# Kernel tuning notes

Measured on AMD Instinct MI355X. Metric: run time of the kernel, lower is better.

## Reference

```python
import jax, jax.numpy as jnp
import numpy as np

B, T, D, N, L = 8, 2048, 256, 64, 4
LN_EPS = 1e-5


def setup_inputs() -> dict:
    key = jax.random.key(0)
    ks = jax.random.split(key, 8)
    def rn(k, shape, scale=1.0):
        return jax.random.normal(k, shape, dtype=jnp.float32) * scale
    A_init = jnp.log(0.5 + jnp.arange(N, dtype=jnp.float32))  # (N,)
    inp = {
        "sequences": rn(ks[0], (B, T, D)),
        # per-layer stacked params (leading dim L)
        "Wi": rn(ks[1], (L, D, D), 1.0 / np.sqrt(D)),
        "bi": jnp.zeros((L, D), jnp.float32),
        "A_log": jnp.broadcast_to(A_init, (L, D, N)) + 0.0,
        "Cm": rn(ks[2], (L, D, N), 1.0 / np.sqrt(N)),
        "Dp": jnp.ones((L, D), jnp.float32),
        "log_dt": jax.random.uniform(ks[3], (L, D), jnp.float32) * (np.log(0.1) - np.log(0.001)) + np.log(0.001),
        "Wo": rn(ks[4], (L, D, D), 1.0 / np.sqrt(D)),
        "bo": jnp.zeros((L, D), jnp.float32),
        "ln1_g": jnp.ones((L, D), jnp.float32),
        "ln1_b": jnp.zeros((L, D), jnp.float32),
        "ln2_g": jnp.ones((L, D), jnp.float32),
        "ln2_b": jnp.zeros((L, D), jnp.float32),
        "W1": rn(ks[5], (L, D, 4 * D), 1.0 / np.sqrt(D)),
        "b1": jnp.zeros((L, 4 * D), jnp.float32),
        "W2": rn(ks[6], (L, 4 * D, D), 1.0 / np.sqrt(4 * D)),
        "b2": jnp.zeros((L, D), jnp.float32),
        "lnf_g": jnp.ones((D,), jnp.float32),
        "lnf_b": jnp.zeros((D,), jnp.float32),
    }
    return inp


def _ln(x, g, b):
    m = x.mean(-1, keepdims=True)
    v = x.var(-1, keepdims=True)
    return (x - m) / jnp.sqrt(v + LN_EPS) * g + b


def _s4_kernel(A_log_l, Cm_l, log_dt_l, Tlen):
    dt = jnp.exp(log_dt_l)                       # (D,)
    A = -jnp.exp(A_log_l)                        # (D,N)
    A_bar = jnp.exp(A * dt[:, None])             # (D,N)
    B_bar = (A_bar - 1.0) / (A * np.sqrt(N))     # (D,N)
    CB = Cm_l * B_bar                            # (D,N)
    logAb = jnp.log(jnp.clip(A_bar, 1e-10))
    powers = jnp.arange(Tlen, dtype=jnp.float32)
    # (D,N,T) power tensor contracted over N -> (D,T)
    return jnp.einsum('dn,dnt->dt', CB, jnp.exp(logAb[:, :, None] * powers))


def reference(sequences, Wi, bi, A_log, Cm, Dp, log_dt, Wo, bo,
              ln1_g, ln1_b, ln2_g, ln2_b, W1, b1, W2, b2, lnf_g, lnf_b):
    x = sequences  # dropout is identity in eval mode
    Tlen = x.shape[1]
    nfft = 2 * Tlen
    for l in range(L):
        # --- S4D sub-block (pre-norm) ---
        h = _ln(x, ln1_g[l], ln1_b[l])
        u = (h @ Wi[l] + bi[l]).transpose(0, 2, 1)   # (B,D,T)
        K = _s4_kernel(A_log[l], Cm[l], log_dt[l], Tlen)  # (D,T)
        u_f = jnp.fft.rfft(u, n=nfft, axis=-1)
        K_f = jnp.fft.rfft(K, n=nfft, axis=-1)
        y = jnp.fft.irfft(u_f * K_f[None], n=nfft, axis=-1)[..., :Tlen]
        y = y + Dp[l][None, :, None] * u
        y = y.transpose(0, 2, 1) @ Wo[l] + bo[l]
        x = x + y
        # --- MLP sub-block (pre-norm) ---
        h2 = _ln(x, ln2_g[l], ln2_b[l])
        x = x + (jax.nn.gelu(h2 @ W1[l] + b1[l], approximate=False) @ W2[l] + b2[l])
    return _ln(x, lnf_g, lnf_b)
```

## Files before the change

kernel.cpp:

```cpp
#include <hip/hip_runtime.h>
#include <hip/hip_bf16.h>

#define NB 8
#define TT 2048
#define DD 256
#define NN 64
#define LL 4
#define CC 32
#define GG 64
#define BT (NB*TT)

typedef __attribute__((ext_vector_type(8))) short short8;
typedef __attribute__((ext_vector_type(4))) short short4v;
typedef __attribute__((ext_vector_type(4))) float f32x4;

__device__ __forceinline__ float bf2f(__hip_bfloat16 v){ return __bfloat162float(v); }
__device__ __forceinline__ __hip_bfloat16 f2bf(float v){ return __float2bfloat16(v); }
__device__ __forceinline__ short f2bfbits(float v){
  __hip_bfloat16 h = __float2bfloat16(v);
  return __builtin_bit_cast(short, h);
}
__device__ __forceinline__ float bfbits2f(short s){
  __hip_bfloat16 h = __builtin_bit_cast(__hip_bfloat16, s);
  return __bfloat162float(h);
}

__device__ __forceinline__ int get_bf(const void* dtp){
  unsigned u = *(const unsigned*)dtp;
  return ((u >> 16) == (u & 0xFFFFu)) ? 1 : 0;
}

__device__ __forceinline__ float ldin(const void* p, size_t i, int bf){
  return bf ? __bfloat162float(((const __hip_bfloat16*)p)[i]) : ((const float*)p)[i];
}

__device__ __forceinline__ float gelu_f(float x){
  float y = 0.79788456f * fmaf(0.044715f, x*x*x, x);
  float e = __expf(-2.0f * fabsf(y));
  float t = (1.0f - e) / (1.0f + e);
  t = (y >= 0.0f) ? t : -t;
  return 0.5f * x * (1.0f + t);
}

__device__ __forceinline__ void async16(const void* g, void* l){
  __builtin_amdgcn_global_load_lds(
      (const __attribute__((address_space(1))) void*)(unsigned long long)g,
      (__attribute__((address_space(3))) void*)(unsigned long long)l,
      16, 0, 0);
}

__global__ __launch_bounds__(256) void cast_ln_kernel(const void* __restrict__ seq,
    __hip_bfloat16* __restrict__ x, __hip_bfloat16* __restrict__ hN,
    const void* __restrict__ g, const void* __restrict__ b,
    const void* __restrict__ dtp)
{
  int bf = get_bf(dtp);
  int lane = threadIdx.x & 63, w = threadIdx.x >> 6;
  int row = blockIdx.x * 4 + w;
  int c = lane * 4;
  size_t base = (size_t)row*DD + c;
  float v0 = ldin(seq, base+0, bf), v1 = ldin(seq, base+1, bf);
  float v2 = ldin(seq, base+2, bf), v3 = ldin(seq, base+3, bf);
  short4v xk; xk.x=f2bfbits(v0); xk.y=f2bfbits(v1); xk.z=f2bfbits(v2); xk.w=f2bfbits(v3);
  *(short4v*)(x + base) = xk;
  float s = v0+v1+v2+v3;
  #pragma unroll
  for (int o = 1; o < 64; o <<= 1) s += __shfl_xor(s, o);
  float mean = s * (1.0f/DD);
  float d0=v0-mean, d1=v1-mean, d2=v2-mean, d3=v3-mean;
  float sq = d0*d0+d1*d1+d2*d2+d3*d3;
  #pragma unroll
  for (int o = 1; o < 64; o <<= 1) sq += __shfl_xor(sq, o);
  float r = rsqrtf(sq * (1.0f/DD) + 1e-5f);
  short4v hk;
  hk.x = f2bfbits(d0*r*ldin(g,c+0,bf) + ldin(b,c+0,bf));
  hk.y = f2bfbits(d1*r*ldin(g,c+1,bf) + ldin(b,c+1,bf));
  hk.z = f2bfbits(d2*r*ldin(g,c+2,bf) + ldin(b,c+2,bf));
  hk.w = f2bfbits(d3*r*ldin(g,c+3,bf) + ldin(b,c+3,bf));
  *(short4v*)(hN + base) = hk;
}

__global__ __launch_bounds__(256) void transpose_all_kernel(
    const void* __restrict__ Wi, const void* __restrict__ Wo,
    const void* __restrict__ W1, const void* __restrict__ W2,
    __hip_bfloat16* __restrict__ WiT, __hip_bfloat16* __restrict__ WoT,
    __hip_bfloat16* __restrict__ W1T, __hip_bfloat16* __restrict__ W2T,
    const void* __restrict__ dtp)
{
  int bf = get_bf(dtp);
  __shared__ float tile[32][33];
  int id = blockIdx.x;
  const void* W; __hip_bfloat16* Wt; int K, N, l, n0, k0;
  if (id < 256){
    W=Wi; Wt=WiT; K=DD; N=DD;
    int t=id;       l=t>>6; int r=t&63;  n0=(r&7)*32;  k0=(r>>3)*32;
  } else if (id < 512){
    W=Wo; Wt=WoT; K=DD; N=DD;
    int t=id-256;   l=t>>6; int r=t&63;  n0=(r&7)*32;  k0=(r>>3)*32;
  } else if (id < 1536){
    W=W1; Wt=W1T; K=DD; N=4*DD;
    int t=id-512;   l=t>>8; int r=t&255; n0=(r&31)*32; k0=(r>>5)*32;
  } else {
    W=W2; Wt=W2T; K=4*DD; N=DD;
    int t=id-1536;  l=t>>8; int r=t&255; n0=(r&7)*32;  k0=(r>>3)*32;
  }
  size_t zoff = (size_t)l * K * N;
  int tx = threadIdx.x, ty = threadIdx.y;
  #pragma unroll
  for (int i = 0; i < 4; i++)
    tile[ty + i*8][tx] = ldin(W, zoff + (size_t)(k0 + ty + i*8)*N + n0 + tx, bf);
  __syncthreads();
  #pragma unroll
  for (int i = 0; i < 4; i++)
    Wt[zoff + (size_t)(n0 + ty + i*8)*K + k0 + tx] = f2bf(tile[tx][ty + i*8]);
}

__global__ __launch_bounds__(256) void gemm_w1_kernel(
    const __hip_bfloat16* __restrict__ A, const __hip_bfloat16* __restrict__ Wt,
    const void* __restrict__ bias, size_t boff,
    __hip_bfloat16* __restrict__ C, int N, int K, const void* __restrict__ dtp)
{
  int bf = get_bf(dtp);
  __shared__ __align__(16) char smem[24576];
  short (*Als)[128][32] = (short(*)[128][32])smem;
  short (*Bls)[64][32]  = (short(*)[64][32])(smem + 16384);
  short* Cls = (short*)smem;
  int tid = threadIdx.x;
  int lane = tid & 63, w = tid >> 6;
  int quad = lane >> 4, row16 = lane & 15;
  int wm = (w >> 1) * 64, wn = (w & 1) * 32;
  int bm = blockIdx.x * 128, bn = blockIdx.y * 64;
  const short* Ag = (const short*)A + (size_t)bm * K;
  const short* Bg = (const short*)Wt + (size_t)bn * K;
  int r0 = tid >> 2, c8 = (tid & 3) * 8;
  f32x4 acc[4][2] = {};
  for (int k0 = 0; k0 < K; k0 += 64){
    #pragma unroll
    for (int kc = 0; kc < 2; kc++){
      async16(Ag + (size_t)r0*K      + k0 + kc*32 + c8, &Als[kc][r0][c8]);
      async16(Ag + (size_t)(64+r0)*K + k0 + kc*32 + c8, &Als[kc][64+r0][c8]);
      async16(Bg + (size_t)r0*K      + k0 + kc*32 + c8, &Bls[kc][r0][c8]);
    }
    __syncthreads();
    #pragma unroll
    for (int kc = 0; kc < 2; kc++){
      short8 af[4], bfr[2];
      #pragma unroll
      for (int i = 0; i < 4; i++)
        af[i] = *(const short8*)&Als[kc][wm + i*16 + row16][quad*8];
      #pragma unroll
      for (int j = 0; j < 2; j++)
        bfr[j] = *(const short8*)&Bls[kc][wn + j*16 + row16][quad*8];
      #pragma unroll
      for (int i = 0; i < 4; i++)
        #pragma unroll
        for (int j = 0; j < 2; j++)
          acc[i][j] = __builtin_amdgcn_mfma_f32_16x16x32_bf16(af[i], bfr[j], acc[i][j], 0, 0, 0);
    }
    __syncthreads();
  }
  #pragma unroll
  for (int i = 0; i < 4; i++){
    #pragma unroll
    for (int j = 0; j < 2; j++){
      int col = wn + j*16 + row16;
      float bv = ldin(bias, boff + bn + col, bf);
      #pragma unroll
      for (int r = 0; r < 4; r++){
        int row = wm + i*16 + quad*4 + r;
        Cls[row*72 + col] = f2bfbits(gelu_f(acc[i][j][r] + bv));
      }
    }
  }
  __syncthreads();
  #pragma unroll
  for (int p = 0; p < 4; p++){
    int ch = p*256 + tid;
    int row = ch >> 3, c0 = (ch & 7) * 8;
    short8 v = *(const short8*)&Cls[row*72 + c0];
    *(short8*)&C[(size_t)(bm + row)*N + bn + c0] = v;
  }
}

__global__ __launch_bounds__(256) void gemm_wi_lf_kernel(
    const __hip_bfloat16* __restrict__ A, const __hip_bfloat16* __restrict__ Wt,
    const void* __restrict__ bias, size_t boff,
    __hip_bfloat16* __restrict__ uout, __hip_bfloat16* __restrict__ LFS,
    const float* __restrict__ abT, int K, const void* __restrict__ dtp)
{
  int bf = get_bf(dtp);
  __shared__ __align__(16) char smem[73728];
  short (*Als)[2][32][32]  = (short(*)[2][32][32])smem;
  short (*Bls)[2][256][32] = (short(*)[2][256][32])(smem + 8192);
  float* Cls = (float*)smem;
  int tid = threadIdx.x, lane = tid & 63, w = tid >> 6;
  int quad = lane >> 4, row16 = lane & 15;
  int wn = w * 64;
  int bm = blockIdx.x * 32;
  const short* Ag = (const short*)A + (size_t)bm * K;
  const short* Bg = (const short*)Wt;
  int nt = K >> 6;
  {
    int ch = tid; int kc = ch>>7, r=(ch>>2)&31, c=(ch&3)*8;
    async16(Ag + (size_t)r*K + kc*32 + c, &Als[0][kc][r][c]);
    #pragma unroll
    for (int p = 0; p < 8; p++){
      int c2 = p*256 + tid; int k2 = c2>>10, r2=(c2>>2)&255, cc=(c2&3)*8;
      async16(Bg + (size_t)r2*K + k2*32 + cc, &Bls[0][k2][r2][cc]);
    }
  }
  __syncthreads();
  f32x4 acc[2][4] = {};
  for (int t = 0; t < nt; t++){
    int cur = t & 1;
    if (t + 1 < nt){
      int nb_ = cur ^ 1, k0 = (t+1) << 6;
      int ch = tid; int kc = ch>>7, r=(ch>>2)&31, c=(ch&3)*8;
      async16(Ag + (size_t)r*K + k0 + kc*32 + c, &Als[nb_][kc][r][c]);
      #pragma unroll
      for (int p = 0; p < 8; p++){
        int c2 = p*256 + tid; int k2 = c2>>10, r2=(c2>>2)&255, cc=(c2&3)*8;
        async16(Bg + (size_t)r2*K + k0 + k2*32 + cc, &Bls[nb_][k2][r2][cc]);
      }
    }
    #pragma unroll
    for (int kc = 0; kc < 2; kc++){
      short8 af[2], bfr[4];
      #pragma unroll
      for (int i = 0; i < 2; i++)
        af[i] = *(const short8*)&Als[cur][kc][i*16 + row16][quad*8];
      #pragma unroll
      for (int j = 0; j < 4; j++)
        bfr[j] = *(const short8*)&Bls[cur][kc][wn + j*16 + row16][quad*8];
      #pragma unroll
      for (int i = 0; i < 2; i++)
        #pragma unroll
        for (int j = 0; j < 4; j++)
          acc[i][j] = __builtin_amdgcn_mfma_f32_16x16x32_bf16(af[i], bfr[j], acc[i][j], 0, 0, 0);
    }
    __syncthreads();
  }
  #pragma unroll
  for (int i = 0; i < 2; i++)
    #pragma unroll
    for (int j = 0; j < 4; j++){
      int col = wn + j*16 + row16;
      #pragma unroll
      for (int r = 0; r < 4; r++){
        int row = i*16 + quad*4 + r;
        Cls[row*260 + col] = acc[i][j][r];
      }
    }
  __syncthreads();
  {
    int row = tid >> 3, l7 = tid & 7;
    size_t rbase = (size_t)(bm + row)*DD;
    #pragma unroll
    for (int q = 0; q < 8; q++){
      int c0 = l7*4 + q*32;
      float4 t = *(const float4*)&Cls[row*260 + c0];
      float v0 = t.x + ldin(bias, boff+c0+0, bf);
      float v1 = t.y + ldin(bias, boff+c0+1, bf);
      float v2 = t.z + ldin(bias, boff+c0+2, bf);
      float v3 = t.w + ldin(bias, boff+c0+3, bf);
      float4 wbk; wbk.x=v0; wbk.y=v1; wbk.z=v2; wbk.w=v3;
      *(float4*)&Cls[row*260 + c0] = wbk;
      short4v pk; pk.x=f2bfbits(v0); pk.y=f2bfbits(v1); pk.z=f2bfbits(v2); pk.w=f2bfbits(v3);
      *(short4v*)&uout[rbase + c0] = pk;
    }
  }
  __syncthreads();
  {
    int d = tid;
    int cix = bm >> 5;
    float ab[NN], accn[NN];
    #pragma unroll
    for (int n = 0; n < NN; n++){ ab[n] = abT[n*DD + d]; accn[n] = 0.0f; }
    #pragma unroll 1
    for (int s = 0; s < CC; s++){
      float uv = Cls[s*260 + d];
      #pragma unroll
      for (int n = 0; n < NN; n++) accn[n] = fmaf(ab[n], accn[n], uv);
    }
    #pragma unroll
    for (int n = 0; n < NN; n++)
      LFS[((size_t)cix*NN + n)*DD + d] = f2bf(accn[n]);
  }
}

__global__ __launch_bounds__(256) void s4_scan_kernel(__hip_bfloat16* __restrict__ LFS,
    const float* __restrict__ AbarCT)
{
  int d = threadIdx.x;
  int n = blockIdx.x & (NN-1), b = blockIdx.x >> 6;
  float a = AbarCT[n*DD + d];
  size_t base = ((size_t)(b*GG)*NN + n)*DD + d;
  const size_t gs = (size_t)NN*DD;
  float s = 0.0f;
  #pragma unroll 1
  for (int g = 0; g < GG; g += 4){
    size_t i0 = base + (size_t)(g+0)*gs;
    size_t i1 = base + (size_t)(g+1)*gs;
    size_t i2 = base + (size_t)(g+2)*gs;
    size_t i3 = base + (size_t)(g+3)*gs;
    float lf0 = bf2f(LFS[i0]);
    float lf1 = bf2f(LFS[i1]);
    float lf2 = bf2f(LFS[i2]);
    float lf3 = bf2f(LFS[i3]);
    LFS[i0] = f2bf(s); s = fmaf(a, s, lf0);
    LFS[i1] = f2bf(s); s = fmaf(a, s, lf1);
    LFS[i2] = f2bf(s); s = fmaf(a, s, lf2);
    LFS[i3] = f2bf(s); s = fmaf(a, s, lf3);
  }
}

__global__ __launch_bounds__(512, 4) void gemm_wo_recur_kernel(
    const __hip_bfloat16* __restrict__ uB, const __hip_bfloat16* __restrict__ Sin,
    const float* __restrict__ abT, const float* __restrict__ cbT,
    const void* __restrict__ Dp, size_t dpoff,
    const __hip_bfloat16* __restrict__ Wt, const void* __restrict__ bias, size_t boff,
    const __hip_bfloat16* __restrict__ resx, __hip_bfloat16* __restrict__ xout,
    const void* __restrict__ g, size_t goff, const void* __restrict__ bb, size_t bboff,
    __hip_bfloat16* __restrict__ hout)
{
  int bf = get_bf(Dp);
  __shared__ __align__(16) char smem[50176];
  short* Uls   = (short*)smem;
  short* Afull = (short*)(smem + 16384);
  short* Bext  = (short*)(smem + 32768);
  float* Cls   = (float*)(smem + 16384);
  int tid = threadIdx.x, lane = tid & 63, w = tid >> 6;
  int quad = lane >> 4, row16 = lane & 15;
  int bm = blockIdx.x * CC;
  const short* Bg = (const short*)Wt;
  {
    const short* ug = (const short*)uB + (size_t)bm * DD;
    async16(ug + tid*8,        Uls + tid*8);
    async16(ug + 4096 + tid*8, Uls + 4096 + tid*8);
    #pragma unroll
    for (int p = 0; p < 2; p++){
      int ch = p*512 + tid; int r = ch >> 2, c = (ch & 3) * 8;
      async16(Bg + (size_t)r*DD + c, Bext + ch*8);
    }
  }
  int d = tid >> 1, ng = tid & 1, nb = ng * 32;
  float st[32], ab[32], cb[32];
  {
    const __hip_bfloat16* sbase = Sin + ((size_t)(bm >> 5) * NN + nb)*DD + d;
    const float* abase = abT + (size_t)nb*DD + d;
    const float* cbase = cbT + (size_t)nb*DD + d;
    #pragma unroll
    for (int i = 0; i < 32; i++){
      st[i] = bf2f(sbase[(size_t)i*DD]);
      ab[i] = abase[(size_t)i*DD];
      cb[i] = cbase[(size_t)i*DD];
    }
  }
  float dp = ldin(Dp, dpoff + d, bf);
  __syncthreads();
  {
    short* ya = Afull + (d >> 5)*1024 + (d & 31);
    float uv = bfbits2f(Uls[d]);
    #pragma unroll 1
    for (int tau = 0; tau < CC; tau++){
      float uvn = (tau < CC-1) ? bfbits2f(Uls[(tau+1)*DD + d]) : 0.0f;
      float a0 = 0.0f, a1 = 0.0f, a2 = 0.0f, a3 = 0.0f;
      #pragma unroll
      for (int i = 0; i < 32; i += 4){
        st[i+0] = fmaf(ab[i+0], st[i+0], uv); a0 = fmaf(cb[i+0], st[i+0], a0);
        st[i+1] = fmaf(ab[i+1], st[i+1], uv); a1 = fmaf(cb[i+1], st[i+1], a1);
        st[i+2] = fmaf(ab[i+2], st[i+2], uv); a2 = fmaf(cb[i+2], st[i+2], a2);
        st[i+3] = fmaf(ab[i+3], st[i+3], uv); a3 = fmaf(cb[i+3], st[i+3], a3);
      }
      float tot = (a0 + a1) + (a2 + a3);
      tot += __shfl_xor(tot, 1);
      if (ng == 0) ya[tau*32] = f2bfbits(fmaf(dp, uv, tot));
      uv = uvn;
    }
  }
  __syncthreads();
  int wn = w * 32;
  f32x4 acc[2][2] = {};
  #pragma unroll
  for (int t = 0; t < 8; t++){
    if (t < 7){
      short* nxt = ((t+1) & 1) ? Uls : Bext;
      #pragma unroll
      for (int p = 0; p < 2; p++){
        int ch = p*512 + tid; int r = ch >> 2, c = (ch & 3) * 8;
        async16(Bg + (size_t)r*DD + (t+1)*32 + c, nxt + ch*8);
      }
    }
    const short* cur = (t & 1) ? Uls : Bext;
    short8 af[2], bfr[2];
    #pragma unroll
    for (int i = 0; i < 2; i++)
      af[i] = *(const short8*)&Afull[t*1024 + (i*16 + row16)*32 + quad*8];
    #pragma unroll
    for (int j = 0; j < 2; j++)
      bfr[j] = *(const short8*)&cur[(wn + j*16 + row16)*32 + quad*8];
    #pragma unroll
    for (int i = 0; i < 2; i++)
      #pragma unroll
      for (int j = 0; j < 2; j++)
        acc[i][j] = __builtin_amdgcn_mfma_f32_16x16x32_bf16(af[i], bfr[j], acc[i][j], 0, 0, 0);
    __syncthreads();
  }
  #pragma unroll
  for (int i = 0; i < 2; i++)
    #pragma unroll
    for (int j = 0; j < 2; j++){
      int col = wn + j*16 + row16;
      #pragma unroll
      for (int r = 0; r < 4; r++){
        int row = i*16 + quad*4 + r;
        Cls[row*260 + col] = acc[i][j][r];
      }
    }
  __syncthreads();
  int row = tid >> 4, l4 = tid & 15;
  size_t rbase = (size_t)(bm + row)*DD;
  float v[4][4];
  #pragma unroll
  for (int q = 0; q < 4; q++){
    int c0 = l4*4 + q*64;
    float4 t = *(const float4*)&Cls[row*260 + c0];
    short4v rx = *(const short4v*)&resx[rbase + c0];
    v[q][0] = t.x + ldin(bias, boff+c0+0, bf) + bfbits2f(rx.x);
    v[q][1] = t.y + ldin(bias, boff+c0+1, bf) + bfbits2f(rx.y);
    v[q][2] = t.z + ldin(bias, boff+c0+2, bf) + bfbits2f(rx.z);
    v[q][3] = t.w + ldin(bias, boff+c0+3, bf) + bfbits2f(rx.w);
    short4v pk; pk.x=f2bfbits(v[q][0]); pk.y=f2bfbits(v[q][1]);
    pk.z=f2bfbits(v[q][2]); pk.w=f2bfbits(v[q][3]);
    *(short4v*)&xout[rbase + c0] = pk;
  }
  float s = 0.0f, sq = 0.0f;
  #pragma unroll
  for (int q = 0; q < 4; q++)
    #pragma unroll
    for (int e = 0; e < 4; e++){ s += v[q][e]; sq += v[q][e]*v[q][e]; }
  #pragma unroll
  for (int o = 1; o < 16; o <<= 1){ s += __shfl_xor(s, o); sq += __shfl_xor(sq, o); }
  float mean = s * (1.0f/DD);
  float rstd = rsqrtf(sq * (1.0f/DD) - mean*mean + 1e-5f);
  #pragma unroll
  for (int q = 0; q < 4; q++){
    int c0 = l4*4 + q*64;
    short4v pk;
    pk.x = f2bfbits((v[q][0]-mean)*rstd*ldin(g,goff+c0+0,bf) + ldin(bb,bboff+c0+0,bf));
    pk.y = f2bfbits((v[q][1]-mean)*rstd*ldin(g,goff+c0+1,bf) + ldin(bb,bboff+c0+1,bf));
    pk.z = f2bfbits((v[q][2]-mean)*rstd*ldin(g,goff+c0+2,bf) + ldin(bb,bboff+c0+2,bf));
    pk.w = f2bfbits((v[q][3]-mean)*rstd*ldin(g,goff+c0+3,bf) + ldin(bb,bboff+c0+3,bf));
    *(short4v*)&hout[rbase + c0] = pk;
  }
}

template <int MODE>
__global__ __launch_bounds__(256) void gemm_row_kernel(
    const __hip_bfloat16* __restrict__ A, const __hip_bfloat16* __restrict__ Wt,
    const void* __restrict__ bias, size_t boff,
    const __hip_bfloat16* __restrict__ resx, __hip_bfloat16* __restrict__ xout,
    const void* __restrict__ g, size_t goff,
    const void* __restrict__ bb, size_t bboff,
    __hip_bfloat16* __restrict__ hout, void* __restrict__ vout,
    int K, const void* __restrict__ dtp)
{
  int bf = get_bf(dtp);
  __shared__ __align__(16) char smem[73728];
  short (*Als)[2][32][32]  = (short(*)[2][32][32])smem;
  short (*Bls)[2][256][32] = (short(*)[2][256][32])(smem + 8192);
  float* Cls = (float*)smem;
  int tid = threadIdx.x, lane = tid & 63, w = tid >> 6;
  int quad = lane >> 4, row16 = lane & 15;
  int wn = w * 64;
  int bm = blockIdx.x * 32;
  const short* Ag = (const short*)A + (size_t)bm * K;
  const short* Bg = (const short*)Wt;
  int nt = K >> 6;
  {
    int ch = tid; int kc = ch>>7, r=(ch>>2)&31, c=(ch&3)*8;
    async16(Ag + (size_t)r*K + kc*32 + c, &Als[0][kc][r][c]);
    #pragma unroll
    for (int p = 0; p < 8; p++){
      int c2 = p*256 + tid; int k2 = c2>>10, r2=(c2>>2)&255, cc=(c2&3)*8;
      async16(Bg + (size_t)r2*K + k2*32 + cc, &Bls[0][k2][r2][cc]);
    }
  }
  __syncthreads();
  f32x4 acc[2][4] = {};
  for (int t = 0; t < nt; t++){
    int cur = t & 1;
    if (t + 1 < nt){
      int nb_ = cur ^ 1, k0 = (t+1) << 6;
      int ch = tid; int kc = ch>>7, r=(ch>>2)&31, c=(ch&3)*8;
      async16(Ag + (size_t)r*K + k0 + kc*32 + c, &Als[nb_][kc][r][c]);
      #pragma unroll
      for (int p = 0; p < 8; p++){
        int c2 = p*256 + tid; int k2 = c2>>10, r2=(c2>>2)&255, cc=(c2&3)*8;
        async16(Bg + (size_t)r2*K + k0 + k2*32 + cc, &Bls[nb_][k2][r2][cc]);
      }
    }
    #pragma unroll
    for (int kc = 0; kc < 2; kc++){
      short8 af[2], bfr[4];
      #pragma unroll
      for (int i = 0; i < 2; i++)
        af[i] = *(const short8*)&Als[cur][kc][i*16 + row16][quad*8];
      #pragma unroll
      for (int j = 0; j < 4; j++)
        bfr[j] = *(const short8*)&Bls[cur][kc][wn + j*16 + row16][quad*8];
      #pragma unroll
      for (int i = 0; i < 2; i++)
        #pragma unroll
        for (int j = 0; j < 4; j++)
          acc[i][j] = __builtin_amdgcn_mfma_f32_16x16x32_bf16(af[i], bfr[j], acc[i][j], 0, 0, 0);
    }
    __syncthreads();
  }
  #pragma unroll
  for (int i = 0; i < 2; i++)
    #pragma unroll
    for (int j = 0; j < 4; j++){
      int col = wn + j*16 + row16;
      #pragma unroll
      for (int r = 0; r < 4; r++){
        int row = i*16 + quad*4 + r;
        Cls[row*260 + col] = acc[i][j][r];
      }
    }
  __syncthreads();
  int row = tid >> 3, l7 = tid & 7;
  size_t rbase = (size_t)(bm + row)*DD;
  float v[8][4];
  #pragma unroll
  for (int q = 0; q < 8; q++){
    int c0 = l7*4 + q*32;
    float4 t = *(const float4*)&Cls[row*260 + c0];
    short4v rx = *(const short4v*)&resx[rbase + c0];
    v[q][0] = t.x + ldin(bias, boff+c0+0, bf) + bfbits2f(rx.x);
    v[q][1] = t.y + ldin(bias, boff+c0+1, bf) + bfbits2f(rx.y);
    v[q][2] = t.z + ldin(bias, boff+c0+2, bf) + bfbits2f(rx.z);
    v[q][3] = t.w + ldin(bias, boff+c0+3, bf) + bfbits2f(rx.w);
    if (MODE == 1){
      short4v pk; pk.x=f2bfbits(v[q][0]); pk.y=f2bfbits(v[q][1]);
      pk.z=f2bfbits(v[q][2]); pk.w=f2bfbits(v[q][3]);
      *(short4v*)&xout[rbase + c0] = pk;
    }
  }
  float s = 0.0f, sq = 0.0f;
  #pragma unroll
  for (int q = 0; q < 8; q++)
    #pragma unroll
    for (int e = 0; e < 4; e++){ s += v[q][e]; sq += v[q][e]*v[q][e]; }
  #pragma unroll
  for (int o = 1; o < 8; o <<= 1){ s += __shfl_xor(s, o); sq += __shfl_xor(sq, o); }
  float mean = s * (1.0f/DD);
  float rstd = rsqrtf(sq * (1.0f/DD) - mean*mean + 1e-5f);
  #pragma unroll
  for (int q = 0; q < 8; q++){
    int c0 = l7*4 + q*32;
    float o0 = (v[q][0]-mean)*rstd*ldin(g,goff+c0+0,bf) + ldin(bb,bboff+c0+0,bf);
    float o1 = (v[q][1]-mean)*rstd*ldin(g,goff+c0+1,bf) + ldin(bb,bboff+c0+1,bf);
    float o2 = (v[q][2]-mean)*rstd*ldin(g,goff+c0+2,bf) + ldin(bb,bboff+c0+2,bf);
    float o3 = (v[q][3]-mean)*rstd*ldin(g,goff+c0+3,bf) + ldin(bb,bboff+c0+3,bf);
    if (MODE == 1){
      short4v pk; pk.x=f2bfbits(o0); pk.y=f2bfbits(o1); pk.z=f2bfbits(o2); pk.w=f2bfbits(o3);
      *(short4v*)&hout[rbase + c0] = pk;
    } else {
      if (bf){
        short4v pk; pk.x=f2bfbits(o0); pk.y=f2bfbits(o1); pk.z=f2bfbits(o2); pk.w=f2bfbits(o3);
        *(short4v*)&((__hip_bfloat16*)vout)[rbase + c0] = pk;
      } else {
        float4 pk; pk.x=o0; pk.y=o1; pk.z=o2; pk.w=o3;
        *(float4*)&((float*)vout)[rbase + c0] = pk;
      }
    }
  }
}

__global__ __launch_bounds__(256) void s4_setup_kernel(const void* __restrict__ A_log,
    const void* __restrict__ Cm, const void* __restrict__ log_dt,
    float* __restrict__ AbarT, float* __restrict__ AbarCT, float* __restrict__ cbT,
    const void* __restrict__ dtp)
{
  int bf = get_bf(dtp);
  int d = threadIdx.x, n = blockIdx.x, l = blockIdx.y;
  float dtv = expf(ldin(log_dt, (size_t)l*DD + d, bf));
  float A   = -expf(ldin(A_log, ((size_t)l*DD + d)*NN + n, bf));
  float ab  = expf(A * dtv);
  float bbv = (fabsf(A) > 1e-8f) ? (ab - 1.0f) / (A * 8.0f) : dtv * 0.125f;
  float cb  = ldin(Cm, ((size_t)l*DD + d)*NN + n, bf) * bbv;
  size_t o = ((size_t)l*NN + n)*DD + d;
  AbarT[o] = ab;
  cbT[o]   = cb;
  float p = ab;
  #pragma unroll
  for (int i = 0; i < 5; i++) p *= p;
  AbarCT[o] = p;
}

extern "C" void kernel_launch(void* const* d_in, const int* in_sizes, int n_in,
                              void* d_out, int out_size, void* d_ws, size_t ws_size,
                              hipStream_t stream) {
  const void* seq   = d_in[0];
  const void* Wi    = d_in[1];
  const void* bi    = d_in[2];
  const void* A_log = d_in[3];
  const void* Cm    = d_in[4];
  const void* Dp    = d_in[5];
  const void* logdt = d_in[6];
  const void* Wo    = d_in[7];
  const void* bo    = d_in[8];
  const void* ln1g  = d_in[9];
  const void* ln1b  = d_in[10];
  const void* ln2g  = d_in[11];
  const void* ln2b  = d_in[12];
  const void* W1    = d_in[13];
  const void* b1    = d_in[14];
  const void* W2    = d_in[15];
  const void* b2    = d_in[16];
  const void* lnfg  = d_in[17];
  const void* lnfb  = d_in[18];

  char* ws = (char*)d_ws;
  size_t off = 0;
  __hip_bfloat16* x   = (__hip_bfloat16*)(ws + off); off += (size_t)BT*DD*2;
  __hip_bfloat16* uB  = (__hip_bfloat16*)(ws + off); off += (size_t)BT*DD*2;
  __hip_bfloat16* hN  = (__hip_bfloat16*)(ws + off); off += (size_t)BT*DD*2;
  __hip_bfloat16* mid = (__hip_bfloat16*)(ws + off); off += (size_t)BT*4*DD*2;
  __hip_bfloat16* LFS = (__hip_bfloat16*)(ws + off); off += (size_t)NB*GG*NN*DD*2;
  __hip_bfloat16* WiT = (__hip_bfloat16*)(ws + off); off += (size_t)LL*DD*DD*2;
  __hip_bfloat16* WoT = (__hip_bfloat16*)(ws + off); off += (size_t)LL*DD*DD*2;
  __hip_bfloat16* W1T = (__hip_bfloat16*)(ws + off); off += (size_t)LL*DD*4*DD*2;
  __hip_bfloat16* W2T = (__hip_bfloat16*)(ws + off); off += (size_t)LL*4*DD*DD*2;
  float* AbarT  = (float*)(ws + off); off += (size_t)LL*NN*DD*4;
  float* AbarCT = (float*)(ws + off); off += (size_t)LL*NN*DD*4;
  float* cbT    = (float*)(ws + off); off += (size_t)LL*NN*DD*4;

  (void)in_sizes; (void)n_in; (void)out_size; (void)ws_size;

  cast_ln_kernel<<<BT/4, 256, 0, stream>>>(seq, x, hN, ln1g, ln1b, Dp);
  transpose_all_kernel<<<2560, dim3(32,8), 0, stream>>>(
      Wi, Wo, W1, W2, WiT, WoT, W1T, W2T, Dp);
  s4_setup_kernel<<<dim3(NN, LL), DD, 0, stream>>>(A_log, Cm, logdt, AbarT, AbarCT, cbT, Dp);

  for (int l = 0; l < LL; l++){
    const size_t oD  = (size_t)l*DD;
    const size_t o4D = (size_t)l*4*DD;
    const float* abT  = AbarT  + (size_t)l*NN*DD;
    const float* abCT = AbarCT + (size_t)l*NN*DD;
    const float* cbTl = cbT    + (size_t)l*NN*DD;

    gemm_wi_lf_kernel<<<BT/32, 256, 0, stream>>>(
        hN, WiT + (size_t)l*DD*DD, bi, oD, uB, LFS, abT, DD, Dp);
    s4_scan_kernel<<<NB*NN, 256, 0, stream>>>(LFS, abCT);
    gemm_wo_recur_kernel<<<BT/32, 512, 0, stream>>>(
        uB, LFS, abT, cbTl, Dp, oD,
        WoT + (size_t)l*DD*DD, bo, oD, x, x,
        ln2g, oD, ln2b, oD, hN);

    gemm_w1_kernel<<<dim3(BT/128, 4*DD/64), 256, 0, stream>>>(
        hN, W1T + (size_t)l*DD*4*DD, b1, o4D, mid, 4*DD, DD, Dp);
    if (l < LL-1){
      gemm_row_kernel<1><<<BT/32, 256, 0, stream>>>(
          mid, W2T + (size_t)l*4*DD*DD, b2, oD, x, x,
          ln1g, (size_t)(l+1)*DD, ln1b, (size_t)(l+1)*DD, hN, nullptr, 4*DD, Dp);
    } else {
      gemm_row_kernel<2><<<BT/32, 256, 0, stream>>>(
          mid, W2T + (size_t)l*4*DD*DD, b2, oD, x, nullptr,
          lnfg, 0, lnfb, 0, nullptr, d_out, 4*DD, Dp);
    }
  }
}
```

Measured before the change: 591.2 us.

## Double-buffer W1 GEMM and use partial vmcnt waits with split barriers

Turns the W1 GEMM into a double-buffered pipeline that prefetches the next K tile while computing the current one, doubling its LDS to 48 KB. Across all the MFMA GEMM loops, the full __syncthreads is replaced by explicit s_waitcnt vmcnt(N) waits that leave only the newest prefetch in flight, plus raw s_barrier calls fenced with sched_barrier. The aim is to keep global loads overlapped with MFMA work instead of draining every outstanding load at each barrier. The risks are the hand-picked vmcnt values, which must match the exact number of async loads issued per thread, and lower occupancy from the larger LDS footprint.

```diff
diff --git a/kernel.cpp b/kernel.cpp
--- a/kernel.cpp
+++ b/kernel.cpp
@@ -23,6 +23,22 @@
 __device__ __forceinline__ float bfbits2f(short s){
   __hip_bfloat16 h = __builtin_bit_cast(__hip_bfloat16, s);
   return __bfloat162float(h);
+}
+
+#define VMCNT(N) do{ asm volatile("s_waitcnt vmcnt(" #N ")" ::: "memory"); \
+                     __builtin_amdgcn_sched_barrier(0); }while(0)
+__device__ __forceinline__ void barrier_pre(){
+  asm volatile("" ::: "memory");
+  __builtin_amdgcn_s_barrier();
+  asm volatile("" ::: "memory");
+  __builtin_amdgcn_sched_barrier(0);
+}
+__device__ __forceinline__ void barrier_post(){
+  asm volatile("s_waitcnt lgkmcnt(0)" ::: "memory");
+  __builtin_amdgcn_sched_barrier(0);
+  __builtin_amdgcn_s_barrier();
+  asm volatile("" ::: "memory");
+  __builtin_amdgcn_sched_barrier(0);
 }
 
 __device__ __forceinline__ int get_bf(const void* dtp){
@@ -121,9 +137,9 @@
     __hip_bfloat16* __restrict__ C, int N, int K, const void* __restrict__ dtp)
 {
   int bf = get_bf(dtp);
-  __shared__ __align__(16) char smem[24576];
-  short (*Als)[128][32] = (short(*)[128][32])smem;
-  short (*Bls)[64][32]  = (short(*)[64][32])(smem + 16384);
+  __shared__ __align__(16) char smem[49152];
+  short (*Als)[2][128][32] = (short(*)[2][128][32])smem;
+  short (*Bls)[2][64][32]  = (short(*)[2][64][32])(smem + 32768);
   short* Cls = (short*)smem;
   int tid = threadIdx.x;
   int lane = tid & 63, w = tid >> 6;
@@ -132,32 +148,55 @@
   int bm = blockIdx.x * 128, bn = blockIdx.y * 64;
   const short* Ag = (const short*)A + (size_t)bm * K;
   const short* Bg = (const short*)Wt + (size_t)bn * K;
-  int r0 = tid >> 2, c8 = (tid & 3) * 8;
+  int nt = K >> 6;
+  {
+    #pragma unroll
+    for (int p = 0; p < 4; p++){
+      int ch = p*256 + tid; int kc = ch>>9, r=(ch>>2)&127, c=(ch&3)*8;
+      async16(Ag + (size_t)r*K + kc*32 + c, &Als[0][kc][r][c]);
+    }
+    #pragma unroll
+    for (int p = 0; p < 2; p++){
+      int c2 = p*256 + tid; int k2 = c2>>8, r2=(c2>>2)&63, cc=(c2&3)*8;
+      async16(Bg + (size_t)r2*K + k2*32 + cc, &Bls[0][k2][r2][cc]);
+    }
+  }
   f32x4 acc[4][2] = {};
-  for (int k0 = 0; k0 < K; k0 += 64){
-    #pragma unroll
-    for (int kc = 0; kc < 2; kc++){
-      async16(Ag + (size_t)r0*K      + k0 + kc*32 + c8, &Als[kc][r0][c8]);
-      async16(Ag + (size_t)(64+r0)*K + k0 + kc*32 + c8, &Als[kc][64+r0][c8]);
-      async16(Bg + (size_t)r0*K      + k0 + kc*32 + c8, &Bls[kc][r0][c8]);
-    }
-    __syncthreads();
+  for (int t = 0; t < nt; t++){
+    int cur = t & 1;
+    if (t + 1 < nt){
+      int nb_ = cur ^ 1, k0 = (t+1) << 6;
+      #pragma unroll
+      for (int p = 0; p < 4; p++){
+        int ch = p*256 + tid; int kc = ch>>9, r=(ch>>2)&127, c=(ch&3)*8;
+        async16(Ag + (size_t)r*K + k0 + kc*32 + c, &Als[nb_][kc][r][c]);
+      }
+      #pragma unroll
+      for (int p = 0; p < 2; p++){
+        int c2 = p*256 + tid; int k2 = c2>>8, r2=(c2>>2)&63, cc=(c2&3)*8;
+        async16(Bg + (size_t)r2*K + k0 + k2*32 + cc, &Bls[nb_][k2][r2][cc]);
+      }
+      VMCNT(6);
+    } else {
+      VMCNT(0);
+    }
+    barrier_pre();
     #pragma unroll
     for (int kc = 0; kc < 2; kc++){
       short8 af[4], bfr[2];
       #pragma unroll
       for (int i = 0; i < 4; i++)
-        af[i] = *(const short8*)&Als[kc][wm + i*16 + row16][quad*8];
+        af[i] = *(const short8*)&Als[cur][kc][wm + i*16 + row16][quad*8];
       #pragma unroll
       for (int j = 0; j < 2; j++)
-        bfr[j] = *(const short8*)&Bls[kc][wn + j*16 + row16][quad*8];
+        bfr[j] = *(const short8*)&Bls[cur][kc][wn + j*16 + row16][quad*8];
       #pragma unroll
       for (int i = 0; i < 4; i++)
         #pragma unroll
         for (int j = 0; j < 2; j++)
           acc[i][j] = __builtin_amdgcn_mfma_f32_16x16x32_bf16(af[i], bfr[j], acc[i][j], 0, 0, 0);
     }
-    __syncthreads();
+    barrier_post();
   }
   #pragma unroll
   for (int i = 0; i < 4; i++){
@@ -209,7 +248,6 @@
       async16(Bg + (size_t)r2*K + k2*32 + cc, &Bls[0][k2][r2][cc]);
     }
   }
-  __syncthreads();
   f32x4 acc[2][4] = {};
   for (int t = 0; t < nt; t++){
     int cur = t & 1;
@@ -222,7 +260,11 @@
         int c2 = p*256 + tid; int k2 = c2>>10, r2=(c2>>2)&255, cc=(c2&3)*8;
         async16(Bg + (size_t)r2*K + k0 + k2*32 + cc, &Bls[nb_][k2][r2][cc]);
       }
-    }
+      VMCNT(9);
+    } else {
+      VMCNT(0);
+    }
+    barrier_pre();
     #pragma unroll
     for (int kc = 0; kc < 2; kc++){
       short8 af[2], bfr[4];
@@ -238,7 +280,7 @@
         for (int j = 0; j < 4; j++)
           acc[i][j] = __builtin_amdgcn_mfma_f32_16x16x32_bf16(af[i], bfr[j], acc[i][j], 0, 0, 0);
     }
-    __syncthreads();
+    barrier_post();
   }
   #pragma unroll
   for (int i = 0; i < 2; i++)
@@ -390,7 +432,11 @@
         int ch = p*512 + tid; int r = ch >> 2, c = (ch & 3) * 8;
         async16(Bg + (size_t)r*DD + (t+1)*32 + c, nxt + ch*8);
       }
-    }
+      VMCNT(2);
+    } else {
+      VMCNT(0);
+    }
+    barrier_pre();
     const short* cur = (t & 1) ? Uls : Bext;
     short8 af[2], bfr[2];
     #pragma unroll
@@ -404,7 +450,7 @@
       #pragma unroll
       for (int j = 0; j < 2; j++)
         acc[i][j] = __builtin_amdgcn_mfma_f32_16x16x32_bf16(af[i], bfr[j], acc[i][j], 0, 0, 0);
-    __syncthreads();
+    barrier_post();
   }
   #pragma unroll
   for (int i = 0; i < 2; i++)
@@ -486,7 +532,6 @@
       async16(Bg + (size_t)r2*K + k2*32 + cc, &Bls[0][k2][r2][cc]);
     }
   }
-  __syncthreads();
   f32x4 acc[2][4] = {};
   for (int t = 0; t < nt; t++){
     int cur = t & 1;
@@ -499,7 +544,11 @@
         int c2 = p*256 + tid; int k2 = c2>>10, r2=(c2>>2)&255, cc=(c2&3)*8;
         async16(Bg + (size_t)r2*K + k0 + k2*32 + cc, &Bls[nb_][k2][r2][cc]);
       }
-    }
+      VMCNT(9);
+    } else {
+      VMCNT(0);
+    }
+    barrier_pre();
     #pragma unroll
     for (int kc = 0; kc < 2; kc++){
       short8 af[2], bfr[4];
@@ -515,7 +564,7 @@
         for (int j = 0; j < 4; j++)
           acc[i][j] = __builtin_amdgcn_mfma_f32_16x16x32_bf16(af[i], bfr[j], acc[i][j], 0, 0, 0);
     }
-    __syncthreads();
+    barrier_post();
   }
   #pragma unroll
   for (int i = 0; i < 2; i++)
```

Result: no change. 589.0 us (-0.4%).
